# Performance work log

Measured on AMD Instinct MI355X. Metric: run time of the kernel, lower is better.

The kernel has to match this reference:

```python
import jax, jax.numpy as jnp
import numpy as np

B, N, IN_F, OUT_F, H = 4, 2048, 128, 128, 4
D = OUT_F // H  # head_dim = 32
NEG_SLOPE = 0.2


def setup_inputs() -> dict:
    key = jax.random.key(0)
    k1, k2, k3, k4, k5 = jax.random.split(key, 5)
    x = jax.random.normal(k1, (B, N, IN_F), dtype=jnp.float32)
    adj = jax.random.randint(k2, (N, N), 0, 2, dtype=jnp.int32)
    adj = adj.at[jnp.arange(N), jnp.arange(N)].set(1)  # self-loops
    # xavier-uniform-like init
    lim_w = float(np.sqrt(6.0 / (IN_F + OUT_F)))
    W = jax.random.uniform(k3, (OUT_F, IN_F), minval=-lim_w, maxval=lim_w, dtype=jnp.float32)
    lim_a = float(np.sqrt(6.0 / (H + D)))
    a_src = jax.random.uniform(k4, (H, D), minval=-lim_a, maxval=lim_a, dtype=jnp.float32)
    a_dst = jax.random.uniform(k5, (H, D), minval=-lim_a, maxval=lim_a, dtype=jnp.float32)
    return {"x": x, "adj": adj, "W": W, "a_src": a_src, "a_dst": a_dst}


def reference(x, adj, W, a_src, a_dst):
    Bx, Nx, _ = x.shape
    # linear projection: (B,N,out) -> (B,N,H,D)
    h = jnp.einsum('bni,oi->bno', x, W).reshape(Bx, Nx, H, D)
    e_src = jnp.einsum('bnhd,hd->bnh', h, a_src)  # (B,N,H)
    e_dst = jnp.einsum('bnhd,hd->bnh', h, a_dst)  # (B,N,H)
    # scores: (B,N_src,H,N_dst)
    scores = jax.nn.leaky_relu(
        e_src[:, :, :, None] + e_dst.transpose(0, 2, 1)[:, None, :, :],
        negative_slope=NEG_SLOPE,
    )
    mask = adj[None, :, None, :]  # (1,N,1,N)
    scores = jnp.where(mask == 0, -jnp.inf, scores)
    attn = jax.nn.softmax(scores, axis=-1)  # (B,N,H,N); dropout is identity at eval
    out = jnp.einsum('bnhm,bmhd->bnhd', attn, h)  # (B,N,H,D)
    return out.reshape(Bx, Nx, H * D)
```

## Files before the change

kernel.cpp:

```cpp
#include <hip/hip_runtime.h>
#include <math.h>

#define BB 4
#define NN 2048
#define FF 128
#define HH 4
#define DD 32
#define NEG_SLOPE 0.2f
#define LOG2E 1.4426950408889634f

typedef __attribute__((ext_vector_type(8))) short short8;
typedef __attribute__((ext_vector_type(4))) float floatx4;
typedef __attribute__((ext_vector_type(2))) float floatx2;

__device__ __forceinline__ float exp2_fast(float x) {
#if __has_builtin(__builtin_amdgcn_exp2f)
    return __builtin_amdgcn_exp2f(x);
#else
    return exp2f(x);
#endif
}

__device__ __forceinline__ int bit_mask(unsigned int w, int bit) {
#if __has_builtin(__builtin_amdgcn_sbfe)
    return __builtin_amdgcn_sbfe((int)w, bit, 1);
#else
    return ((int)(w << (31 - bit))) >> 31;
#endif
}

__device__ __forceinline__ unsigned short to_bf16(float f) {
    unsigned int ui = __float_as_uint(f);
    ui += 0x7FFFu + ((ui >> 16) & 1u);
    return (unsigned short)(ui >> 16);
}

__global__ __launch_bounds__(256) void k_prep(const float* __restrict__ x,
                                              const float* __restrict__ W,
                                              const float* __restrict__ a_src,
                                              const float* __restrict__ a_dst,
                                              const int* __restrict__ adj,
                                              unsigned short* __restrict__ ht,
                                              float* __restrict__ es_t,
                                              float* __restrict__ ed_t,
                                              unsigned int* __restrict__ bits) {
    __shared__ float xs[16][FF];
    __shared__ float wt[32][132];
    __shared__ float as_s[FF], ad_s[FF];
    __shared__ unsigned short tile2[16][136];
    int t = threadIdx.x;

    if (blockIdx.x >= 512) {
        int idx = (blockIdx.x - 512) * 256 + t;
        int n = idx >> 6, w = idx & 63;
        const int4* base = (const int4*)(adj + (size_t)n * NN + w * 32);
        unsigned int word = 0;
#pragma unroll
        for (int q = 0; q < 8; ++q) {
            int4 a = base[q];
            word |= ((unsigned int)(a.x & 1)) << (q * 4 + 0);
            word |= ((unsigned int)(a.y & 1)) << (q * 4 + 1);
            word |= ((unsigned int)(a.z & 1)) << (q * 4 + 2);
            word |= ((unsigned int)(a.w & 1)) << (q * 4 + 3);
        }
        bits[idx] = word;
        return;
    }

    long rows0 = (long)blockIdx.x * 16;
    if (t < FF) { as_s[t] = a_src[t]; ad_s[t] = a_dst[t]; }
#pragma unroll
    for (int k = 0; k < 2; ++k) {
        int q = t + k * 256;
        int r = q >> 5, c4 = q & 31;
        float4 v = ((const float4*)(x + (rows0 + r) * FF))[c4];
        *(float4*)&xs[r][c4 * 4] = v;
    }
    int og = t & 31, rg = t >> 5;
    float acc[2][4];
#pragma unroll
    for (int a = 0; a < 2; ++a)
#pragma unroll
        for (int c = 0; c < 4; ++c) acc[a][c] = 0.f;

    int wo = t & 127, wg = t >> 7;
    for (int i0 = 0; i0 < FF; i0 += 32) {
        __syncthreads();
#pragma unroll
        for (int u = 0; u < 4; ++u) {
            float4 v = *(const float4*)(W + (long)wo * FF + i0 + wg * 16 + u * 4);
            wt[wg * 16 + u * 4 + 0][wo] = v.x;
            wt[wg * 16 + u * 4 + 1][wo] = v.y;
            wt[wg * 16 + u * 4 + 2][wo] = v.z;
            wt[wg * 16 + u * 4 + 3][wo] = v.w;
        }
        __syncthreads();
#pragma unroll
        for (int i = 0; i < 32; ++i) {
            float4 w4 = *(const float4*)&wt[i][og * 4];
            float x0 = xs[rg * 2 + 0][i0 + i];
            float x1 = xs[rg * 2 + 1][i0 + i];
            acc[0][0] += x0 * w4.x; acc[0][1] += x0 * w4.y;
            acc[0][2] += x0 * w4.z; acc[0][3] += x0 * w4.w;
            acc[1][0] += x1 * w4.x; acc[1][1] += x1 * w4.y;
            acc[1][2] += x1 * w4.z; acc[1][3] += x1 * w4.w;
        }
    }

    int head = og >> 3;
    int b = (int)(rows0 >> 11);
    int m_block = (int)(rows0 & 2047);
    float es0 = 0.f, ed0 = 0.f, es1 = 0.f, ed1 = 0.f;
#pragma unroll
    for (int c = 0; c < 4; ++c) {
        int col = og * 4 + c;
        es0 += acc[0][c] * as_s[col]; ed0 += acc[0][c] * ad_s[col];
        es1 += acc[1][c] * as_s[col]; ed1 += acc[1][c] * ad_s[col];
    }
#pragma unroll
    for (int k = 1; k < 8; k <<= 1) {
        es0 += __shfl_xor(es0, k); ed0 += __shfl_xor(ed0, k);
        es1 += __shfl_xor(es1, k); ed1 += __shfl_xor(ed1, k);
    }
    if ((og & 7) == 0) {
        size_t eb = (size_t)(b * HH + head) * NN + m_block + rg * 2;
        es_t[eb]     = es0 * LOG2E; ed_t[eb]     = ed0 * LOG2E;
        es_t[eb + 1] = es1 * LOG2E; ed_t[eb + 1] = ed1 * LOG2E;
    }

#pragma unroll
    for (int a = 0; a < 2; ++a)
#pragma unroll
        for (int c = 0; c < 4; ++c)
            tile2[rg * 2 + a][og * 4 + c] = to_bf16(acc[a][c]);
    __syncthreads();
    {
        int cg = t >> 1, half = t & 1;
        int d = cg & 31, hd = cg >> 5;
        unsigned short tmp[8];
#pragma unroll
        for (int j = 0; j < 8; ++j) tmp[j] = tile2[half * 8 + j][cg];
        unsigned short* op = ht + ((size_t)(b * HH + hd) * DD + d) * NN + m_block + half * 8;
        *(int4*)op = *(const int4*)tmp;
    }
}

#define HTS 2056
__global__ __launch_bounds__(1024) void k_attn(
        const unsigned short* __restrict__ ht,
        const unsigned int* __restrict__ bits,
        const float* __restrict__ es_t,
        const float* __restrict__ ed_t,
        float* __restrict__ out) {
    __shared__ unsigned short hb[DD * HTS];
    __shared__ float ep[NN * 2];
    int t = threadIdx.x;
    int n0 = blockIdx.x * 128;
    int bh = blockIdx.y;
    int b = bh >> 2, head = bh & 3;

    int wid = t >> 6, lane = t & 63;
    int q = lane >> 4, r = lane & 15;
    int qo = q * 8;
    int half = wid >> 3, wsub = wid & 7;
    int n_l = wsub * 16 + r;

    {
        float2 v = ((const float2*)(ed_t + (size_t)bh * NN))[t];
        float4 o;
        o.x = exp2_fast(v.x); o.y = exp2_fast(NEG_SLOPE * v.x);
        o.z = exp2_fast(v.y); o.w = exp2_fast(NEG_SLOPE * v.y);
        ((float4*)ep)[t] = o;
    }
    {
        const unsigned short* htp = ht + (size_t)bh * DD * NN;
#pragma unroll
        for (int k = 0; k < 8; ++k) {
            int qq = t + k * 1024;
            int d = qq >> 8, cm = qq & 255;
            int4 v = *(const int4*)(htp + (size_t)d * NN + cm * 8);
            *(int4*)&hb[d * HTS + cm * 8] = v;
        }
    }
    int4 bw[8];
    {
        const int4* bp = (const int4*)(bits + (size_t)(n0 + n_l) * 64 + half * 32);
#pragma unroll
        for (int g = 0; g < 8; ++g) bw[g] = bp[g];
    }
    float esv = es_t[(size_t)bh * NN + n0 + n_l];
    floatx2 es2 = {exp2_fast(esv), exp2_fast(NEG_SLOPE * esv)};
    __syncthreads();

    floatx4 acc0 = {0.f, 0.f, 0.f, 0.f};
    floatx4 acc1 = {0.f, 0.f, 0.f, 0.f};
    floatx4 accd = {0.f, 0.f, 0.f, 0.f};
    union { short8 s8; int i[4]; } ones;
    ones.i[0] = 0x3F803F80; ones.i[1] = 0x3F803F80;
    ones.i[2] = 0x3F803F80; ones.i[3] = 0x3F803F80;

    const float* eph = ep + half * 2048;
    const unsigned short* hrow0 = &hb[r * HTS + half * 1024 + qo];
    const unsigned short* hrow1 = hrow0 + 16 * HTS;

#pragma unroll
    for (int g = 0; g < 8; ++g) {
#pragma unroll
        for (int c = 0; c < 4; ++c) {
            unsigned int word = (unsigned int)((&bw[g].x)[c]);
            int mb = (g * 4 + c) * 32;
            unsigned int wq = word >> qo;
            const float* pbase = eph + (mb + qo) * 2;
            union { short8 s8; int i[4]; } af;
#pragma unroll
            for (int jp = 0; jp < 4; ++jp) {
                float4 d2 = *(const float4*)(pbase + jp * 4);
                floatx2 p0 = es2 * (floatx2){d2.x, d2.y};
                floatx2 p1 = es2 * (floatx2){d2.z, d2.w};
                float w0 = fmaxf(p0.x, p0.y);
                float w1 = fmaxf(p1.x, p1.y);
                int m0 = bit_mask(wq, 2 * jp);
                int m1 = bit_mask(wq, 2 * jp + 1);
                w0 = __uint_as_float(__float_as_uint(w0) & (unsigned int)m0);
                w1 = __uint_as_float(__float_as_uint(w1) & (unsigned int)m1);
                af.i[jp] = __builtin_amdgcn_perm(__float_as_uint(w1),
                                                 __float_as_uint(w0),
                                                 0x07060302u);
            }
            short8 b0 = *(const short8*)(hrow0 + mb);
            short8 b1 = *(const short8*)(hrow1 + mb);
            acc0 = __builtin_amdgcn_mfma_f32_16x16x32_bf16(af.s8, b0, acc0, 0, 0, 0);
            acc1 = __builtin_amdgcn_mfma_f32_16x16x32_bf16(af.s8, b1, acc1, 0, 0, 0);
            accd = __builtin_amdgcn_mfma_f32_16x16x32_bf16(af.s8, ones.s8, accd, 0, 0, 0);
        }
    }

    __syncthreads();
    float* scr = (float*)hb;
    if (wid >= 8) {
        int base = ((wid - 8) * 64 + lane) * 12;
        *(floatx4*)&scr[base + 0] = acc0;
        *(floatx4*)&scr[base + 4] = acc1;
        *(floatx4*)&scr[base + 8] = accd;
    }
    __syncthreads();
    if (wid < 8) {
        int base = (wid * 64 + lane) * 12;
        floatx4 p0 = *(const floatx4*)&scr[base + 0];
        floatx4 p1 = *(const floatx4*)&scr[base + 4];
        floatx4 pd = *(const floatx4*)&scr[base + 8];
#pragma unroll
        for (int k = 0; k < 4; ++k) {
            acc0[k] += p0[k]; acc1[k] += p1[k]; accd[k] += pd[k];
        }
#pragma unroll
        for (int reg = 0; reg < 4; ++reg) {
            int nrow = n0 + wsub * 16 + q * 4 + reg;
            float inv = 1.0f / accd[reg];
            float* op = out + ((size_t)(b * NN + nrow)) * FF + head * DD;
            op[r]      = acc0[reg] * inv;
            op[16 + r] = acc1[reg] * inv;
        }
    }
}

extern "C" void kernel_launch(void* const* d_in, const int* in_sizes, int n_in,
                              void* d_out, int out_size, void* d_ws, size_t ws_size,
                              hipStream_t stream) {
    const float* x     = (const float*)d_in[0];
    const int*   adj   = (const int*)d_in[1];
    const float* W     = (const float*)d_in[2];
    const float* a_src = (const float*)d_in[3];
    const float* a_dst = (const float*)d_in[4];
    float* out = (float*)d_out;

    float* es_t = (float*)d_ws;
    float* ed_t = es_t + (size_t)BB * HH * NN;
    unsigned int* bits = (unsigned int*)(ed_t + (size_t)BB * HH * NN);
    unsigned short* ht = (unsigned short*)(bits + (size_t)NN * (NN / 32));

    hipLaunchKernelGGL(k_prep, dim3(1024), dim3(256), 0, stream,
                       x, W, a_src, a_dst, adj, ht, es_t, ed_t, bits);
    hipLaunchKernelGGL(k_attn, dim3(NN / 128, BB * HH), dim3(1024), 0, stream,
                       ht, bits, es_t, ed_t, out);
}
```

Before: 102.5 us.

## Switch attention matmul to 32x32x16 MFMA with four-way key split

Replaces the 16x16x32 bf16 MFMA tiling, where two accumulators covered the 32 head dims and the key range was split in half across waves, with 32x32x16 MFMA covering all 32 dims in one accumulator. Waves now take 32 query rows and one quarter of the keys, and the partial results from three waves are reduced through shared memory. This cuts the count of MFMA instructions and of B-operand loads per key chunk. In exchange the denominator MFMA is now as costly as the main one, accumulator register use rises, and the cross-wave reduction is larger.

Result: slower. 105.8 us (+3.2%).

```diff
diff --git a/kernel.cpp b/kernel.cpp
--- a/kernel.cpp
+++ b/kernel.cpp
@@ -10,6 +10,7 @@
 #define LOG2E 1.4426950408889634f
 
 typedef __attribute__((ext_vector_type(8))) short short8;
+typedef __attribute__((ext_vector_type(16))) float floatx16;
 typedef __attribute__((ext_vector_type(4))) float floatx4;
 typedef __attribute__((ext_vector_type(2))) float floatx2;
 
@@ -160,10 +161,10 @@
     int b = bh >> 2, head = bh & 3;
 
     int wid = t >> 6, lane = t & 63;
-    int q = lane >> 4, r = lane & 15;
-    int qo = q * 8;
-    int half = wid >> 3, wsub = wid & 7;
-    int n_l = wsub * 16 + r;
+    int nl = lane & 31;
+    int oct = lane >> 5;
+    int ng = wid & 3, ks = wid >> 2;
+    int n_row = n0 + ng * 32 + nl;
 
     {
         float2 v = ((const float2*)(ed_t + (size_t)bh * NN))[t];
@@ -182,84 +183,85 @@
             *(int4*)&hb[d * HTS + cm * 8] = v;
         }
     }
-    int4 bw[8];
-    {
-        const int4* bp = (const int4*)(bits + (size_t)(n0 + n_l) * 64 + half * 32);
-#pragma unroll
-        for (int g = 0; g < 8; ++g) bw[g] = bp[g];
-    }
-    float esv = es_t[(size_t)bh * NN + n0 + n_l];
+    int4 bw[4];
+    {
+        const int4* bp = (const int4*)(bits + (size_t)n_row * 64 + ks * 16);
+#pragma unroll
+        for (int g = 0; g < 4; ++g) bw[g] = bp[g];
+    }
+    float esv = es_t[(size_t)bh * NN + n_row];
     floatx2 es2 = {exp2_fast(esv), exp2_fast(NEG_SLOPE * esv)};
     __syncthreads();
 
-    floatx4 acc0 = {0.f, 0.f, 0.f, 0.f};
-    floatx4 acc1 = {0.f, 0.f, 0.f, 0.f};
-    floatx4 accd = {0.f, 0.f, 0.f, 0.f};
+    floatx16 acc, accd;
+#pragma unroll
+    for (int k = 0; k < 16; ++k) { acc[k] = 0.f; accd[k] = 0.f; }
     union { short8 s8; int i[4]; } ones;
     ones.i[0] = 0x3F803F80; ones.i[1] = 0x3F803F80;
     ones.i[2] = 0x3F803F80; ones.i[3] = 0x3F803F80;
 
-    const float* eph = ep + half * 2048;
-    const unsigned short* hrow0 = &hb[r * HTS + half * 1024 + qo];
-    const unsigned short* hrow1 = hrow0 + 16 * HTS;
-
-#pragma unroll
-    for (int g = 0; g < 8; ++g) {
-#pragma unroll
-        for (int c = 0; c < 4; ++c) {
-            unsigned int word = (unsigned int)((&bw[g].x)[c]);
-            int mb = (g * 4 + c) * 32;
-            unsigned int wq = word >> qo;
-            const float* pbase = eph + (mb + qo) * 2;
-            union { short8 s8; int i[4]; } af;
-#pragma unroll
-            for (int jp = 0; jp < 4; ++jp) {
-                float4 d2 = *(const float4*)(pbase + jp * 4);
-                floatx2 p0 = es2 * (floatx2){d2.x, d2.y};
-                floatx2 p1 = es2 * (floatx2){d2.z, d2.w};
-                float w0 = fmaxf(p0.x, p0.y);
-                float w1 = fmaxf(p1.x, p1.y);
-                int m0 = bit_mask(wq, 2 * jp);
-                int m1 = bit_mask(wq, 2 * jp + 1);
-                w0 = __uint_as_float(__float_as_uint(w0) & (unsigned int)m0);
-                w1 = __uint_as_float(__float_as_uint(w1) & (unsigned int)m1);
-                af.i[jp] = __builtin_amdgcn_perm(__float_as_uint(w1),
-                                                 __float_as_uint(w0),
-                                                 0x07060302u);
+    const float* pq = ep + (size_t)(ks * 512 + oct * 8) * 2;
+    const unsigned short* hrow = &hb[(size_t)nl * HTS + ks * 512 + oct * 8];
+    int shift = oct * 8;
+
+#pragma unroll
+    for (int it = 0; it < 32; ++it) {
+        unsigned int word = (unsigned int)((&bw[it >> 3].x)[(it >> 1) & 3]);
+        unsigned int wq = word >> (((it & 1) << 4) + shift);
+        const float* pb = pq + it * 32;
+        union { short8 s8; int i[4]; } af;
+#pragma unroll
+        for (int jp = 0; jp < 4; ++jp) {
+            float4 d2 = *(const float4*)(pb + jp * 4);
+            floatx2 p0 = es2 * (floatx2){d2.x, d2.y};
+            floatx2 p1 = es2 * (floatx2){d2.z, d2.w};
+            float w0 = fmaxf(p0.x, p0.y);
+            float w1 = fmaxf(p1.x, p1.y);
+            int m0 = bit_mask(wq, 2 * jp);
+            int m1 = bit_mask(wq, 2 * jp + 1);
+            w0 = __uint_as_float(__float_as_uint(w0) & (unsigned int)m0);
+            w1 = __uint_as_float(__float_as_uint(w1) & (unsigned int)m1);
+            af.i[jp] = __builtin_amdgcn_perm(__float_as_uint(w1),
+                                             __float_as_uint(w0),
+                                             0x07060302u);
+        }
+        short8 bf = *(const short8*)(hrow + it * 16);
+        acc  = __builtin_amdgcn_mfma_f32_32x32x16_bf16(af.s8, bf, acc, 0, 0, 0);
+        accd = __builtin_amdgcn_mfma_f32_32x32x16_bf16(af.s8, ones.s8, accd, 0, 0, 0);
+    }
+
+    __syncthreads();
+    float* scr = (float*)hb;
+    if (ks > 0) {
+        int base = ((((ks - 1) * 4 + ng) * 64) + lane) * 32;
+#pragma unroll
+        for (int k2 = 0; k2 < 4; ++k2) {
+            float4 v0 = {acc[k2 * 4], acc[k2 * 4 + 1], acc[k2 * 4 + 2], acc[k2 * 4 + 3]};
+            float4 v1 = {accd[k2 * 4], accd[k2 * 4 + 1], accd[k2 * 4 + 2], accd[k2 * 4 + 3]};
+            *(float4*)&scr[base + k2 * 4] = v0;
+            *(float4*)&scr[base + 16 + k2 * 4] = v1;
+        }
+    }
+    __syncthreads();
+    if (ks == 0) {
+#pragma unroll
+        for (int s = 0; s < 3; ++s) {
+            int base = (((s * 4 + ng) * 64) + lane) * 32;
+#pragma unroll
+            for (int k2 = 0; k2 < 4; ++k2) {
+                float4 v0 = *(const float4*)&scr[base + k2 * 4];
+                float4 v1 = *(const float4*)&scr[base + 16 + k2 * 4];
+                acc[k2 * 4 + 0] += v0.x; acc[k2 * 4 + 1] += v0.y;
+                acc[k2 * 4 + 2] += v0.z; acc[k2 * 4 + 3] += v0.w;
+                accd[k2 * 4 + 0] += v1.x; accd[k2 * 4 + 1] += v1.y;
+                accd[k2 * 4 + 2] += v1.z; accd[k2 * 4 + 3] += v1.w;
             }
-            short8 b0 = *(const short8*)(hrow0 + mb);
-            short8 b1 = *(const short8*)(hrow1 + mb);
-            acc0 = __builtin_amdgcn_mfma_f32_16x16x32_bf16(af.s8, b0, acc0, 0, 0, 0);
-            acc1 = __builtin_amdgcn_mfma_f32_16x16x32_bf16(af.s8, b1, acc1, 0, 0, 0);
-            accd = __builtin_amdgcn_mfma_f32_16x16x32_bf16(af.s8, ones.s8, accd, 0, 0, 0);
-        }
-    }
-
-    __syncthreads();
-    float* scr = (float*)hb;
-    if (wid >= 8) {
-        int base = ((wid - 8) * 64 + lane) * 12;
-        *(floatx4*)&scr[base + 0] = acc0;
-        *(floatx4*)&scr[base + 4] = acc1;
-        *(floatx4*)&scr[base + 8] = accd;
-    }
-    __syncthreads();
-    if (wid < 8) {
-        int base = (wid * 64 + lane) * 12;
-        floatx4 p0 = *(const floatx4*)&scr[base + 0];
-        floatx4 p1 = *(const floatx4*)&scr[base + 4];
-        floatx4 pd = *(const floatx4*)&scr[base + 8];
-#pragma unroll
-        for (int k = 0; k < 4; ++k) {
-            acc0[k] += p0[k]; acc1[k] += p1[k]; accd[k] += pd[k];
-        }
-#pragma unroll
-        for (int reg = 0; reg < 4; ++reg) {
-            int nrow = n0 + wsub * 16 + q * 4 + reg;
+        }
+#pragma unroll
+        for (int reg = 0; reg < 16; ++reg) {
+            int nrow = n0 + ng * 32 + (reg & 3) + 8 * (reg >> 2) + 4 * oct;
             float inv = 1.0f / accd[reg];
-            float* op = out + ((size_t)(b * NN + nrow)) * FF + head * DD;
-            op[r]      = acc0[reg] * inv;
-            op[16 + r] = acc1[reg] * inv;
+            out[((size_t)(b * NN + nrow)) * FF + head * DD + nl] = acc[reg] * inv;
         }
     }
 }
```

## Use bf16 MFMA for projection in k_prep and fold attention vectors into W

Applied to the files above, without the earlier changes.

The fp32 scalar LDS-tiled projection in k_prep becomes a bf16 MFMA 16x16x32 GEMM. W is converted to bf16 in shared memory and x fragments are packed on the fly. The e_src/e_dst scores now come from precomputed vectors W^T·a, dotted with the fp32 x rows, instead of reducing the projected h. This cuts the scalar FMA work in the prep kernel, but every block recomputes the full W conversion and the folded vectors, and the bf16 W used for the folded vectors changes numerics slightly.

After: 101.8 us. Within noise of the previous version (-0.7%).

```diff
diff --git a/kernel.cpp b/kernel.cpp
--- a/kernel.cpp
+++ b/kernel.cpp
@@ -33,6 +33,12 @@
     unsigned int ui = __float_as_uint(f);
     ui += 0x7FFFu + ((ui >> 16) & 1u);
     return (unsigned short)(ui >> 16);
+}
+
+__device__ __forceinline__ unsigned int pack2_rtne(float lo, float hi) {
+    unsigned int ul = __float_as_uint(lo); ul += 0x7FFFu + ((ul >> 16) & 1u);
+    unsigned int uh = __float_as_uint(hi); uh += 0x7FFFu + ((uh >> 16) & 1u);
+    return (ul >> 16) | (uh & 0xFFFF0000u);
 }
 
 __global__ __launch_bounds__(256) void k_prep(const float* __restrict__ x,
@@ -44,10 +50,10 @@
                                               float* __restrict__ es_t,
                                               float* __restrict__ ed_t,
                                               unsigned int* __restrict__ bits) {
-    __shared__ float xs[16][FF];
-    __shared__ float wt[32][132];
+    __shared__ unsigned short wbf[128][144];
+    __shared__ unsigned short hbf[128][24];
+    __shared__ float vs_s[HH][FF], vd_s[HH][FF];
     __shared__ float as_s[FF], ad_s[FF];
-    __shared__ unsigned short tile2[16][136];
     int t = threadIdx.x;
 
     if (blockIdx.x >= 512) {
@@ -67,81 +73,103 @@
         return;
     }
 
-    long rows0 = (long)blockIdx.x * 16;
+    int m0g = blockIdx.x * 16;
+    int b = m0g >> 11;
+    int m_block = m0g & 2047;
+
     if (t < FF) { as_s[t] = a_src[t]; ad_s[t] = a_dst[t]; }
 #pragma unroll
-    for (int k = 0; k < 2; ++k) {
-        int q = t + k * 256;
-        int r = q >> 5, c4 = q & 31;
-        float4 v = ((const float4*)(x + (rows0 + r) * FF))[c4];
-        *(float4*)&xs[r][c4 * 4] = v;
-    }
-    int og = t & 31, rg = t >> 5;
-    float acc[2][4];
-#pragma unroll
-    for (int a = 0; a < 2; ++a)
-#pragma unroll
-        for (int c = 0; c < 4; ++c) acc[a][c] = 0.f;
-
-    int wo = t & 127, wg = t >> 7;
-    for (int i0 = 0; i0 < FF; i0 += 32) {
-        __syncthreads();
-#pragma unroll
-        for (int u = 0; u < 4; ++u) {
-            float4 v = *(const float4*)(W + (long)wo * FF + i0 + wg * 16 + u * 4);
-            wt[wg * 16 + u * 4 + 0][wo] = v.x;
-            wt[wg * 16 + u * 4 + 1][wo] = v.y;
-            wt[wg * 16 + u * 4 + 2][wo] = v.z;
-            wt[wg * 16 + u * 4 + 3][wo] = v.w;
-        }
-        __syncthreads();
-#pragma unroll
-        for (int i = 0; i < 32; ++i) {
-            float4 w4 = *(const float4*)&wt[i][og * 4];
-            float x0 = xs[rg * 2 + 0][i0 + i];
-            float x1 = xs[rg * 2 + 1][i0 + i];
-            acc[0][0] += x0 * w4.x; acc[0][1] += x0 * w4.y;
-            acc[0][2] += x0 * w4.z; acc[0][3] += x0 * w4.w;
-            acc[1][0] += x1 * w4.x; acc[1][1] += x1 * w4.y;
-            acc[1][2] += x1 * w4.z; acc[1][3] += x1 * w4.w;
-        }
-    }
-
-    int head = og >> 3;
-    int b = (int)(rows0 >> 11);
-    int m_block = (int)(rows0 & 2047);
-    float es0 = 0.f, ed0 = 0.f, es1 = 0.f, ed1 = 0.f;
-#pragma unroll
-    for (int c = 0; c < 4; ++c) {
-        int col = og * 4 + c;
-        es0 += acc[0][c] * as_s[col]; ed0 += acc[0][c] * ad_s[col];
-        es1 += acc[1][c] * as_s[col]; ed1 += acc[1][c] * ad_s[col];
-    }
-#pragma unroll
-    for (int k = 1; k < 8; k <<= 1) {
-        es0 += __shfl_xor(es0, k); ed0 += __shfl_xor(ed0, k);
-        es1 += __shfl_xor(es1, k); ed1 += __shfl_xor(ed1, k);
-    }
-    if ((og & 7) == 0) {
-        size_t eb = (size_t)(b * HH + head) * NN + m_block + rg * 2;
-        es_t[eb]     = es0 * LOG2E; ed_t[eb]     = ed0 * LOG2E;
-        es_t[eb + 1] = es1 * LOG2E; ed_t[eb + 1] = ed1 * LOG2E;
-    }
-
-#pragma unroll
-    for (int a = 0; a < 2; ++a)
-#pragma unroll
-        for (int c = 0; c < 4; ++c)
-            tile2[rg * 2 + a][og * 4 + c] = to_bf16(acc[a][c]);
-    __syncthreads();
-    {
-        int cg = t >> 1, half = t & 1;
-        int d = cg & 31, hd = cg >> 5;
-        unsigned short tmp[8];
-#pragma unroll
-        for (int j = 0; j < 8; ++j) tmp[j] = tile2[half * 8 + j][cg];
-        unsigned short* op = ht + ((size_t)(b * HH + hd) * DD + d) * NN + m_block + half * 8;
-        *(int4*)op = *(const int4*)tmp;
+    for (int k = 0; k < 8; ++k) {
+        int idx = t + k * 256;
+        int row = idx >> 4, ch = idx & 15;
+        const float* wp = W + (size_t)row * FF + ch * 8;
+        float4 v0 = *(const float4*)wp;
+        float4 v1 = *(const float4*)(wp + 4);
+        unsigned int u[4];
+        u[0] = pack2_rtne(v0.x, v0.y); u[1] = pack2_rtne(v0.z, v0.w);
+        u[2] = pack2_rtne(v1.x, v1.y); u[3] = pack2_rtne(v1.z, v1.w);
+        *(int4*)&wbf[row][ch * 8] = *(const int4*)u;
+    }
+    __syncthreads();
+
+    {
+        int i = t & 127;
+        float acc4[4] = {0.f, 0.f, 0.f, 0.f};
+        if (t < 128) {
+            for (int o = 0; o < 128; ++o) {
+                float wv = __uint_as_float(((unsigned int)wbf[o][i]) << 16);
+                acc4[o >> 5] += wv * as_s[o];
+            }
+#pragma unroll
+            for (int hd = 0; hd < 4; ++hd) vs_s[hd][i] = acc4[hd];
+        } else {
+            for (int o = 0; o < 128; ++o) {
+                float wv = __uint_as_float(((unsigned int)wbf[o][i]) << 16);
+                acc4[o >> 5] += wv * ad_s[o];
+            }
+#pragma unroll
+            for (int hd = 0; hd < 4; ++hd) vd_s[hd][i] = acc4[hd];
+        }
+    }
+
+    int wid = t >> 6, lane = t & 63;
+    int r = lane & 15, q = lane >> 4;
+    floatx4 acc[2] = {{0.f,0.f,0.f,0.f},{0.f,0.f,0.f,0.f}};
+    const float* xrow = x + (size_t)(m0g + r) * FF + q * 8;
+#pragma unroll
+    for (int kk = 0; kk < 4; ++kk) {
+        float4 a0 = *(const float4*)(xrow + kk * 32);
+        float4 a1 = *(const float4*)(xrow + kk * 32 + 4);
+        union { short8 s8; unsigned int u[4]; } af;
+        af.u[0] = pack2_rtne(a0.x, a0.y); af.u[1] = pack2_rtne(a0.z, a0.w);
+        af.u[2] = pack2_rtne(a1.x, a1.y); af.u[3] = pack2_rtne(a1.z, a1.w);
+#pragma unroll
+        for (int c = 0; c < 2; ++c) {
+            int o = (wid * 2 + c) * 16 + r;
+            short8 bf = *(const short8*)&wbf[o][kk * 32 + q * 8];
+            acc[c] = __builtin_amdgcn_mfma_f32_16x16x32_bf16(af.s8, bf, acc[c], 0, 0, 0);
+        }
+    }
+#pragma unroll
+    for (int c = 0; c < 2; ++c) {
+        int o = (wid * 2 + c) * 16 + r;
+        unsigned int u2[2];
+        u2[0] = pack2_rtne(acc[c][0], acc[c][1]);
+        u2[1] = pack2_rtne(acc[c][2], acc[c][3]);
+        *(int2*)&hbf[o][q * 4] = *(const int2*)u2;
+    }
+    __syncthreads();
+
+    if (t < 128) {
+        int hd = t >> 5, d = t & 31;
+        unsigned short* op = ht + ((size_t)(b * HH + hd) * DD + d) * NN + m_block;
+        *(int4*)op       = *(const int4*)&hbf[t][0];
+        *(int4*)(op + 8) = *(const int4*)&hbf[t][8];
+    }
+    {
+        int m = t >> 4, sg = t & 15;
+        const float* xp = x + (size_t)(m0g + m) * FF + sg * 8;
+        float4 x0 = *(const float4*)xp;
+        float4 x1 = *(const float4*)(xp + 4);
+#pragma unroll
+        for (int hd = 0; hd < 4; ++hd) {
+            const float* vsp = &vs_s[hd][sg * 8];
+            const float* vdp = &vd_s[hd][sg * 8];
+            float es = x0.x * vsp[0] + x0.y * vsp[1] + x0.z * vsp[2] + x0.w * vsp[3]
+                     + x1.x * vsp[4] + x1.y * vsp[5] + x1.z * vsp[6] + x1.w * vsp[7];
+            float ed = x0.x * vdp[0] + x0.y * vdp[1] + x0.z * vdp[2] + x0.w * vdp[3]
+                     + x1.x * vdp[4] + x1.y * vdp[5] + x1.z * vdp[6] + x1.w * vdp[7];
+#pragma unroll
+            for (int k = 1; k < 16; k <<= 1) {
+                es += __shfl_xor(es, k);
+                ed += __shfl_xor(ed, k);
+            }
+            if (sg == 0) {
+                size_t eb = (size_t)(b * HH + hd) * NN + m_block + m;
+                es_t[eb] = es * LOG2E;
+                ed_t[eb] = ed * LOG2E;
+            }
+        }
     }
 }
 
```
